# Kernel tuning notes

Measured on AMD Instinct MI355X. Metric: run time of the kernel, lower is better.

Reference implementation:

```python
import jax, jax.numpy as jnp
import numpy as np

B, S, D, H, HD = 2, 2048, 2048, 16, 128
MAX_TIMESCALE = 10000.0


def _fixed_pos_embedding(features, length, max_timescale):
    # flaxformer embedding.generate_fixed_pos_embedding
    fraction = jnp.arange(0, features, 2, dtype=jnp.float32) / features
    timescale = max_timescale ** fraction  # min_timescale = 1.0
    sinusoid = jnp.einsum('i,j->ij', jnp.arange(length, dtype=jnp.float32), 1.0 / timescale)
    sinusoid = jnp.concatenate([sinusoid, sinusoid], axis=-1)  # [length, features]
    return jnp.sin(sinusoid), jnp.cos(sinusoid)


def _rotate_half(x):
    x1, x2 = jnp.split(x, 2, axis=-1)
    return jnp.concatenate([-x2, x1], axis=-1)


def _apply_rope(x, sin, cos):
    # x: [B, S, H, HD]; sin/cos: [S, HD]
    sin = sin[None, :, None, :].astype(x.dtype)
    cos = cos[None, :, None, :].astype(x.dtype)
    return x * cos + _rotate_half(x) * sin


def setup_inputs() -> dict:
    key = jax.random.key(0)
    ks = jax.random.split(key, 6)
    inputs_q = jax.random.normal(ks[0], (B, S, D), dtype=jnp.float32)
    inputs_kv = jax.random.normal(ks[1], (B, S, D), dtype=jnp.float32)
    scale = D ** -0.5
    wq = jax.random.normal(ks[2], (D, H, HD), dtype=jnp.float32) * scale
    wk = jax.random.normal(ks[3], (D, H, HD), dtype=jnp.float32) * scale
    wv = jax.random.normal(ks[4], (D, H, HD), dtype=jnp.float32) * scale
    wo = jax.random.normal(ks[5], (H, HD, D), dtype=jnp.float32) * ((H * HD) ** -0.5)
    mask = jnp.tril(jnp.ones((S, S), dtype=bool))[None, None]  # causal [1,1,S,S]
    return {"inputs_q": inputs_q, "inputs_kv": inputs_kv, "wq": wq, "wk": wk,
            "wv": wv, "wo": wo, "mask": mask}


def reference(inputs_q, inputs_kv, wq, wk, wv, wo, mask):
    # QKV projections (split-head kernels) -> [B, S, H, HD]
    q = jnp.einsum('bqd,dhf->bqhf', inputs_q, wq)
    k = jnp.einsum('bkd,dhf->bkhf', inputs_kv, wk)
    v = jnp.einsum('bkd,dhf->bkhf', inputs_kv, wv)

    # Rotary embeddings applied to full head dim (fraction_to_rotate = 1.0)
    sin, cos = _fixed_pos_embedding(HD, S, MAX_TIMESCALE)
    q = _apply_rope(q, sin, cos)
    k = _apply_rope(k, sin, cos)

    # Logit rescaling by 1/sqrt(head_dim) (rescale_logits=False default path)
    q = q * (HD ** -0.5)

    logits = jnp.einsum('bqhf,bkhf->bhqk', q, k)  # [B, H, S, S]
    logits = jnp.where(mask, logits, jnp.asarray(-1e10, logits.dtype))
    probs = jax.nn.softmax(logits, axis=-1)

    ctx = jnp.einsum('bhqk,bkhf->bqhf', probs, v)
    out = jnp.einsum('bqhf,hfd->bqd', ctx, wo)  # output projection
    return out
```

## Files before the change

### kernel.cpp

```cpp
#include <hip/hip_runtime.h>

#define S_LEN 2048
#define NH 16
#define HDIM 128
#define DMODEL 2048

typedef __attribute__((ext_vector_type(8))) short bf16x8;
typedef __attribute__((ext_vector_type(4))) float f32x4;

using gas_cvp = const __attribute__((address_space(1))) void*;
using las_vp  = __attribute__((address_space(3))) void*;

__device__ __forceinline__ unsigned short f2bf(float x) {
  unsigned int u = __builtin_bit_cast(unsigned int, x);
  u += 0x7FFFu + ((u >> 16) & 1u);
  return (unsigned short)(u >> 16);
}
__device__ __forceinline__ float bf2f(unsigned short u) {
  unsigned int x = ((unsigned int)u) << 16;
  return __builtin_bit_cast(float, x);
}
__device__ __forceinline__ unsigned int cvt_pk_bf16(float lo, float hi) {
  unsigned int r;
  asm("v_cvt_pk_bf16_f32 %0, %1, %2" : "=v"(r) : "v"(lo), "v"(hi));
  return r;
}

__global__ __launch_bounds__(256) void cvt2_kernel(const float4* __restrict__ inq,
                                                   const float4* __restrict__ inkv,
                                                   ushort4* __restrict__ outq,
                                                   ushort4* __restrict__ outkv, int n4) {
  const float4* in = blockIdx.z ? inkv : inq;
  ushort4* out = blockIdx.z ? outkv : outq;
  int i = blockIdx.x * 256 + threadIdx.x;
  if (i < n4) {
    float4 v = in[i];
    ushort4 r;
    r.x = f2bf(v.x); r.y = f2bf(v.y); r.z = f2bf(v.z); r.w = f2bf(v.w);
    out[i] = r;
  }
}

__global__ __launch_bounds__(256) void sincos_kernel(float2* __restrict__ sc) {
  int i = blockIdx.x * 256 + threadIdx.x;
  int s = i >> 6, j = i & 63;
  float inv_ts = 1.0f / powf(10000.0f, (float)j * (1.0f / 64.0f));
  float ang = (float)s * inv_ts;
  sc[i] = make_float2(sinf(ang), cosf(ang));
}

__global__ __launch_bounds__(256) void rope8_kernel(const unsigned short* __restrict__ XQ,
                                                    const unsigned short* __restrict__ XK,
                                                    const float2* __restrict__ sc,
                                                    unsigned short* __restrict__ outQ,
                                                    unsigned short* __restrict__ outK,
                                                    float qscale) {
  const unsigned short* X = blockIdx.z ? XK : XQ;
  unsigned short* out = blockIdx.z ? outK : outQ;
  float scale = blockIdx.z ? 1.0f : qscale;
  int i = blockIdx.x * 256 + threadIdx.x;
  int m = i >> 7;
  int r = i & 127;
  int h = r >> 3, jb = (r & 7) * 8;
  int s = m & (S_LEN - 1);
  size_t base = (size_t)m * DMODEL + h * HDIM + jb;
  int4 x1 = *(const int4*)(X + base);
  int4 x2 = *(const int4*)(X + base + 64);
  const float2* pp = sc + s * 64 + jb;
  int4 o1, o2;
  int* x1w = (int*)&x1; int* x2w = (int*)&x2;
  int* o1w = (int*)&o1; int* o2w = (int*)&o2;
#pragma unroll
  for (int w = 0; w < 4; w++) {
    float a_lo = bf2f((unsigned short)(x1w[w] & 0xffff));
    float a_hi = bf2f((unsigned short)((unsigned int)x1w[w] >> 16));
    float b_lo = bf2f((unsigned short)(x2w[w] & 0xffff));
    float b_hi = bf2f((unsigned short)((unsigned int)x2w[w] >> 16));
    float2 c0 = pp[w * 2], c1 = pp[w * 2 + 1];
    float r1l = (a_lo * c0.y - b_lo * c0.x) * scale;
    float r1h = (a_hi * c1.y - b_hi * c1.x) * scale;
    float r2l = (b_lo * c0.y + a_lo * c0.x) * scale;
    float r2h = (b_hi * c1.y + a_hi * c1.x) * scale;
    o1w[w] = (int)(cvt_pk_bf16(r1l, r1h));
    o2w[w] = (int)(cvt_pk_bf16(r2l, r2h));
  }
  *(int4*)(out + base) = o1;
  *(int4*)(out + base + 64) = o2;
}

__global__ __launch_bounds__(256) void wtrans4_kernel(const float* __restrict__ w0,
                                                      const float* __restrict__ w1,
                                                      const float* __restrict__ w2,
                                                      const float* __restrict__ w3,
                                                      unsigned short* __restrict__ outb) {
  __shared__ float tile[64][65];
  int z = blockIdx.z;
  const float* in = (z == 0) ? w0 : (z == 1) ? w1 : (z == 2) ? w2 : w3;
  unsigned short* out = outb + (size_t)z * DMODEL * DMODEL;
  int c0 = blockIdx.x * 64, r0 = blockIdx.y * 64;
  int tx = threadIdx.x & 63, ty = threadIdx.x >> 6;
#pragma unroll
  for (int i = 0; i < 16; i++) {
    int r = ty + i * 4;
    tile[r][tx] = in[(size_t)(r0 + r) * DMODEL + c0 + tx];
  }
  __syncthreads();
#pragma unroll
  for (int i = 0; i < 16; i++) {
    int c = ty + i * 4;
    out[(size_t)(c0 + c) * DMODEL + r0 + tx] = f2bf(tile[tx][c]);
  }
}

__global__ __launch_bounds__(256) void vtrans_kernel(const unsigned short* __restrict__ vf,
                                                     unsigned short* __restrict__ Vt) {
  __shared__ unsigned short tile[64][65];
  int z = blockIdx.z; int b = z >> 4, h = z & 15;
  const unsigned short* I = vf + (size_t)b * S_LEN * DMODEL + h * HDIM;
  unsigned short* O = Vt + (size_t)z * HDIM * S_LEN;
  int s0 = blockIdx.y * 64, f0 = blockIdx.x * 64;
  int tx = threadIdx.x & 63, ty = threadIdx.x >> 6;
#pragma unroll
  for (int i = 0; i < 16; i++) {
    int r = ty + i * 4;
    tile[r][tx] = I[(size_t)(s0 + r) * DMODEL + f0 + tx];
  }
  __syncthreads();
#pragma unroll
  for (int i = 0; i < 16; i++) {
    int c = ty + i * 4;
    O[(size_t)(f0 + c) * S_LEN + s0 + tx] = tile[tx][c];
  }
}

__global__ __launch_bounds__(512, 1) void gemm256o_kernel(
    const unsigned short* __restrict__ Aq,
    const unsigned short* __restrict__ Akv,
    const unsigned short* __restrict__ W,
    unsigned short* __restrict__ Cb) {
  constexpr int M = 4096, N = 2048, K = 2048, NT = K / 64;
  __shared__ char lds[131072];
  int wid = blockIdx.z * 128 + blockIdx.y * 8 + blockIdx.x;
  int nid = (wid & 7) * 32 + (wid >> 3);
  int z = nid >> 7;
  int rem = nid & 127;
  int bm = (rem >> 3) * 256, bn = (rem & 7) * 256;
  const unsigned short* A = (z == 0) ? Aq : Akv;
  const unsigned short* Bt = W + (size_t)z * N * K;

  int tid = threadIdx.x, wave = tid >> 6, lane = tid & 63;
  int lr = lane & 15, lq = lane >> 4;
  int wr = wave >> 2, wc = wave & 3;

  auto STAGE_P = [&](int t, int buf, int isB) {
    int k0 = t * 64;
    const unsigned short* src = isB ? Bt : A;
    int rbase = isB ? bn : bm;
    char* dst0 = lds + buf * 65536 + isB * 32768;
#pragma unroll
    for (int i = 0; i < 4; i++) {
      int o = i * 8192 + tid * 16;
      int row = o >> 7, colb = o & 127;
      int sc = colb ^ ((row & 7) << 4);
      __builtin_amdgcn_global_load_lds(
          (gas_cvp)(src + (size_t)(rbase + row) * K + k0 + (sc >> 1)),
          (las_vp)(dst0 + i * 8192 + wave * 1024), 16, 0, 0);
    }
  };
  auto LDA1 = [&](int buf, int m, int kk) -> bf16x8 {
    int row = wr * 128 + m * 16 + lr;
    return *(const bf16x8*)(lds + buf * 65536 + row * 128 +
                            (((kk * 4 + lq) ^ (row & 7)) << 4));
  };
  auto LDB1 = [&](int buf, int n, int kk) -> bf16x8 {
    int row = wc * 64 + n * 16 + lr;
    return *(const bf16x8*)(lds + buf * 65536 + 32768 + row * 128 +
                            (((kk * 4 + lq) ^ (row & 7)) << 4));
  };

  f32x4 acc[8][4] = {};
  bf16x8 aA[4][2], bB[4][2];

  auto OCT = [&](int P, int Q, int sb) {
#pragma unroll
    for (int kk = 0; kk < 2; kk++)
#pragma unroll
      for (int s = 0; s < 2; s++)
#pragma unroll
        for (int nn = 0; nn < 2; nn++)
          acc[2 * P + s][2 * Q + nn] = __builtin_amdgcn_mfma_f32_16x16x32_bf16(
              aA[sb + s][kk], bB[2 * Q + nn][kk], acc[2 * P + s][2 * Q + nn], 0, 0, 0);
  };
  auto RD_A2 = [&](int buf, int m0, int sb) {
#pragma unroll
    for (int kk = 0; kk < 2; kk++)
#pragma unroll
      for (int s = 0; s < 2; s++) aA[sb + s][kk] = LDA1(buf, m0 + s, kk);
  };
  auto RD_B2 = [&](int buf, int n0) {
#pragma unroll
    for (int kk = 0; kk < 2; kk++)
#pragma unroll
      for (int s = 0; s < 2; s++) bB[n0 + s][kk] = LDB1(buf, n0 + s, kk);
  };

  STAGE_P(0, 0, 0); STAGE_P(0, 0, 1);
  asm volatile("s_waitcnt vmcnt(0)" ::: "memory");
  __builtin_amdgcn_sched_barrier(0);

  for (int T = 0; T < NT; T++) {
    int c = T & 1, nc = c ^ 1;
    __builtin_amdgcn_s_barrier();
    if (T + 1 < NT) { STAGE_P(T + 1, nc, 0); STAGE_P(T + 1, nc, 1); }
    __builtin_amdgcn_sched_barrier(0);
    RD_A2(c, 0, 0);
    __builtin_amdgcn_sched_barrier(0);
    RD_B2(c, 0);
    __builtin_amdgcn_sched_barrier(0);
    RD_B2(c, 2);
    __builtin_amdgcn_sched_barrier(0);
    RD_A2(c, 2, 2);
    __builtin_amdgcn_sched_barrier(0);

    asm volatile("s_waitcnt lgkmcnt(8)" ::: "memory");
    __builtin_amdgcn_sched_barrier(0);
    __builtin_amdgcn_s_setprio(1);
    OCT(0, 0, 0);
    __builtin_amdgcn_s_setprio(0);
    asm volatile("s_waitcnt lgkmcnt(4)" ::: "memory");
    __builtin_amdgcn_sched_barrier(0);
    __builtin_amdgcn_s_setprio(1);
    OCT(0, 1, 0);
    __builtin_amdgcn_s_setprio(0);
    RD_A2(c, 4, 0);
    __builtin_amdgcn_sched_barrier(0);
    asm volatile("s_waitcnt lgkmcnt(4)" ::: "memory");
    __builtin_amdgcn_sched_barrier(0);
    __builtin_amdgcn_s_setprio(1);
    OCT(1, 0, 2); OCT(1, 1, 2);
    __builtin_amdgcn_s_setprio(0);
    RD_A2(c, 6, 2);
    __builtin_amdgcn_sched_barrier(0);
    asm volatile("s_waitcnt lgkmcnt(4)" ::: "memory");
    __builtin_amdgcn_sched_barrier(0);
    __builtin_amdgcn_s_setprio(1);
    OCT(2, 0, 0); OCT(2, 1, 0);
    __builtin_amdgcn_s_setprio(0);
    asm volatile("s_waitcnt lgkmcnt(0)" ::: "memory");
    __builtin_amdgcn_sched_barrier(0);
    __builtin_amdgcn_s_setprio(1);
    OCT(3, 0, 2); OCT(3, 1, 2);
    __builtin_amdgcn_s_setprio(0);
    if (T + 1 < NT) {
      asm volatile("s_waitcnt vmcnt(0)" ::: "memory");
      __builtin_amdgcn_sched_barrier(0);
    }
  }
  asm volatile("s_waitcnt vmcnt(0) lgkmcnt(0)" ::: "memory");

  unsigned short* C = Cb + (size_t)z * M * N;
#pragma unroll
  for (int m = 0; m < 8; m++)
#pragma unroll
    for (int n = 0; n < 4; n++) {
      int row0 = bm + wr * 128 + m * 16 + lq * 4;
      int col = bn + wc * 64 + n * 16 + lr;
#pragma unroll
      for (int r = 0; r < 4; r++)
        C[(size_t)(row0 + r) * N + col] = f2bf(acc[m][n][r]);
    }
}

template <bool BF16OUT>
__global__ __launch_bounds__(512, 1) void gemmk_kernel(
    const unsigned short* __restrict__ Aq,
    const unsigned short* __restrict__ Akv,
    const unsigned short* __restrict__ W,
    void* __restrict__ Cb) {
  constexpr int M = 4096, N = 2048, K = 2048, NT = K / 64;
  __shared__ char lds[147456];
  int z = blockIdx.z;
  const unsigned short* A = (z == 0) ? Aq : Akv;
  const unsigned short* Bt = W + (size_t)z * N * K;

  int wid = blockIdx.y * 16 + blockIdx.x;
  int nid = (wid & 7) * 32 + (wid >> 3);
  int bn = (nid & 15) * 128, bm = (nid >> 4) * 256;

  int tid = threadIdx.x, wave = tid >> 6, lane = tid & 63;
  int lr = lane & 15, lq = lane >> 4;
  int wr = wave >> 1, wc = wave & 1;

  auto STAGE_U = [&](int t, int buf, int which) {
    int k0 = t * 64;
    const unsigned short* src = (which < 2) ? A : Bt;
    int rbase = (which < 2) ? (bm + which * 128) : bn;
    char* dst0 = lds + buf * 49152 + which * 16384;
#pragma unroll
    for (int i = 0; i < 2; i++) {
      int o = i * 8192 + wave * 1024 + lane * 16;
      int row = o >> 7, colb = o & 127;
      int sc = colb ^ ((row & 7) << 4);
      __builtin_amdgcn_global_load_lds(
          (gas_cvp)(src + (size_t)(rbase + row) * K + k0 + (sc >> 1)),
          (las_vp)(dst0 + i * 8192 + wave * 1024), 16, 0, 0);
    }
  };
  auto LDA = [&](int buf, int m, int kk) -> bf16x8 {
    int row = wr * 64 + m * 16 + lr;
    int half = row >> 7, r = row & 127;
    int byt = r * 128 + (((kk * 4 + lq) ^ (r & 7)) << 4);
    return *(const bf16x8*)(lds + buf * 49152 + half * 16384 + byt);
  };
  auto LDB = [&](int buf, int n, int kk) -> bf16x8 {
    int row = wc * 64 + n * 16 + lr;
    int byt = row * 128 + (((kk * 4 + lq) ^ (row & 7)) << 4);
    return *(const bf16x8*)(lds + buf * 49152 + 32768 + byt);
  };

  f32x4 acc[4][4] = {};
  bf16x8 aA[4][2], bB[4][2];

  auto QUAD = [&](int mg, int ng) {
#pragma unroll
    for (int kk = 0; kk < 2; kk++)
#pragma unroll
      for (int mm = 0; mm < 2; mm++)
#pragma unroll
        for (int nn = 0; nn < 2; nn++)
          acc[mg * 2 + mm][ng * 2 + nn] = __builtin_amdgcn_mfma_f32_16x16x32_bf16(
              aA[mg * 2 + mm][kk], bB[ng * 2 + nn][kk], acc[mg * 2 + mm][ng * 2 + nn], 0, 0, 0);
  };

  auto BODY = [&](int T, int cur, int dst, int mode) {
    __builtin_amdgcn_s_barrier();
    if (mode == 0) {
      STAGE_U(T + 2, dst, 0); STAGE_U(T + 2, dst, 1); STAGE_U(T + 2, dst, 2);
    }
    __builtin_amdgcn_sched_barrier(0);
#pragma unroll
    for (int kk = 0; kk < 2; kk++)
#pragma unroll
      for (int mm = 0; mm < 2; mm++) aA[mm][kk] = LDA(cur, mm, kk);
#pragma unroll
    for (int kk = 0; kk < 2; kk++)
#pragma unroll
      for (int nn = 0; nn < 2; nn++) bB[nn][kk] = LDB(cur, nn, kk);
    __builtin_amdgcn_sched_barrier(0);
#pragma unroll
    for (int kk = 0; kk < 2; kk++)
#pragma unroll
      for (int nn = 0; nn < 2; nn++) bB[2 + nn][kk] = LDB(cur, 2 + nn, kk);
    __builtin_amdgcn_sched_barrier(0);
#pragma unroll
    for (int kk = 0; kk < 2; kk++)
#pragma unroll
      for (int mm = 0; mm < 2; mm++) aA[2 + mm][kk] = LDA(cur, 2 + mm, kk);
    __builtin_amdgcn_sched_barrier(0);

    asm volatile("s_waitcnt lgkmcnt(8)" ::: "memory");
    __builtin_amdgcn_sched_barrier(0);
    __builtin_amdgcn_s_setprio(1);
    QUAD(0, 0);
    __builtin_amdgcn_s_setprio(0);
    asm volatile("s_waitcnt lgkmcnt(4)" ::: "memory");
    __builtin_amdgcn_sched_barrier(0);
    __builtin_amdgcn_s_setprio(1);
    QUAD(0, 1);
    __builtin_amdgcn_s_setprio(0);
    asm volatile("s_waitcnt lgkmcnt(0)" ::: "memory");
    __builtin_amdgcn_sched_barrier(0);
    __builtin_amdgcn_s_setprio(1);
    QUAD(1, 0); QUAD(1, 1);
    __builtin_amdgcn_s_setprio(0);
    if (mode == 0)      asm volatile("s_waitcnt vmcnt(6)" ::: "memory");
    else if (mode == 1) asm volatile("s_waitcnt vmcnt(0)" ::: "memory");
    __builtin_amdgcn_sched_barrier(0);
  };

  STAGE_U(0, 0, 0); STAGE_U(0, 0, 1); STAGE_U(0, 0, 2);
  STAGE_U(1, 1, 0); STAGE_U(1, 1, 1); STAGE_U(1, 1, 2);
  asm volatile("s_waitcnt vmcnt(6)" ::: "memory");
  __builtin_amdgcn_sched_barrier(0);

  int cur = 0;
  for (int T = 0; T < NT - 2; T++) {
    int dst = (cur == 0) ? 2 : cur - 1;
    BODY(T, cur, dst, 0);
    cur = (cur == 2) ? 0 : cur + 1;
  }
  BODY(NT - 2, cur, 0, 1);
  cur = (cur == 2) ? 0 : cur + 1;
  BODY(NT - 1, cur, 0, 2);
  asm volatile("s_waitcnt vmcnt(0) lgkmcnt(0)" ::: "memory");

#pragma unroll
  for (int m = 0; m < 4; m++)
#pragma unroll
    for (int n = 0; n < 4; n++) {
      int row0 = bm + wr * 64 + m * 16 + lq * 4;
      int col = bn + wc * 64 + n * 16 + lr;
      if (BF16OUT) {
        unsigned short* C = (unsigned short*)Cb;
#pragma unroll
        for (int r = 0; r < 4; r++)
          C[(size_t)(row0 + r) * N + col] = f2bf(acc[m][n][r]);
      } else {
        float* C = (float*)Cb;
#pragma unroll
        for (int r = 0; r < 4; r++)
          C[(size_t)(row0 + r) * N + col] = acc[m][n][r];
      }
    }
}

__global__ __launch_bounds__(512, 1) void attn_kernel(const unsigned short* __restrict__ Qb,
                                                      const unsigned short* __restrict__ Kb,
                                                      const unsigned short* __restrict__ Vt,
                                                      unsigned short* __restrict__ ctx) {
  __shared__ char lds[65536];
  int d = blockIdx.x + 8 * (blockIdx.y + 16 * blockIdx.z);
  int jlo = (d >> 3) & 7;
  int hb = (d & 7) * 4 + (d >> 6);
  int h = hb & 15, b = hb >> 4;

  int tid = threadIdx.x, wave = tid >> 6, lane = tid & 63;
  int lr = lane & 15, lq = lane >> 4;
  int grp = wave >> 2, wsub = wave & 3;
  int qtile = grp ? (15 - jlo) : jlo;
  int qw = qtile * 128 + wsub * 32;
  int nt = 2 * (15 - jlo) + 2;

  const unsigned short* Qp = Qb + (size_t)b * S_LEN * DMODEL + (size_t)h * HDIM;
  const unsigned short* Kp = Kb + (size_t)b * S_LEN * DMODEL + (size_t)h * HDIM;
  const unsigned short* Vp = Vt + (size_t)(b * NH + h) * HDIM * S_LEN;

  bf16x8 qa[2][4];
#pragma unroll
  for (int mi = 0; mi < 2; mi++)
#pragma unroll
    for (int kf = 0; kf < 4; kf++)
      qa[mi][kf] = *(const bf16x8*)(Qp + (size_t)(qw + mi * 16 + lr) * DMODEL + kf * 32 + lq * 8);

  f32x4 o[2][8] = {};
  float mrow[2] = {-1e30f, -1e30f};
  float lsum[2] = {0.f, 0.f};

  auto STAGE = [&](int tt, int bsel) {
    int kk0 = tt * 64;
#pragma unroll
    for (int i = 0; i < 2; i++) {
      int o_ = wave * 2048 + i * 1024 + lane * 16;
      int row = o_ >> 8, colb = o_ & 255;
      int sc_ = colb ^ ((row & 7) << 4);
      __builtin_amdgcn_global_load_lds(
          (gas_cvp)(Kp + (size_t)(kk0 + row) * DMODEL + (sc_ >> 1)),
          (las_vp)(lds + bsel * 32768 + wave * 2048 + i * 1024), 16, 0, 0);
    }
#pragma unroll
    for (int i = 0; i < 2; i++) {
      int o_ = wave * 2048 + i * 1024 + lane * 16;
      int row = o_ >> 7, colb = o_ & 127;
      int sc_ = colb ^ ((row & 7) << 4);
      __builtin_amdgcn_global_load_lds(
          (gas_cvp)(Vp + (size_t)row * S_LEN + kk0 + (sc_ >> 1)),
          (las_vp)(lds + bsel * 32768 + 16384 + wave * 2048 + i * 1024), 16, 0, 0);
    }
  };

  STAGE(0, 0);
  __syncthreads();

  for (int t = 0; t < nt; t++) {
    int cur = t & 1;
    int k0 = t * 64;
    if (t + 1 < nt) STAGE(t + 1, cur ^ 1);

    bool active = (k0 <= qw + 31);
    if (active) {
      const char* kbb = lds + cur * 32768;
      f32x4 sf[2][4] = {};
#pragma unroll
      for (int kf = 0; kf < 4; kf++) {
        bf16x8 kbf[4];
#pragma unroll
        for (int nf = 0; nf < 4; nf++) {
          int row = nf * 16 + lr;
          int colb = kf * 64 + lq * 16;
          kbf[nf] = *(const bf16x8*)(kbb + row * 256 + (colb ^ ((row & 7) << 4)));
        }
#pragma unroll
        for (int nf = 0; nf < 4; nf++)
#pragma unroll
          for (int mi = 0; mi < 2; mi++)
            sf[mi][nf] = __builtin_amdgcn_mfma_f32_16x16x32_bf16(kbf[nf], qa[mi][kf], sf[mi][nf], 0, 0, 0);
      }

      if (k0 + 63 > qw) {
#pragma unroll
        for (int mi = 0; mi < 2; mi++) {
          int q = qw + mi * 16 + lr;
#pragma unroll
          for (int nf = 0; nf < 4; nf++)
#pragma unroll
            for (int r = 0; r < 4; r++)
              if (k0 + nf * 16 + lq * 4 + r > q) sf[mi][nf][r] = -1e30f;
        }
      }

      float vmax[2];
#pragma unroll
      for (int mi = 0; mi < 2; mi++) {
        float v = sf[mi][0][0];
#pragma unroll
        for (int nf = 0; nf < 4; nf++)
#pragma unroll
          for (int r = 0; r < 4; r++) v = fmaxf(v, sf[mi][nf][r]);
        v = fmaxf(v, __shfl_xor(v, 16));
        v = fmaxf(v, __shfl_xor(v, 32));
        vmax[mi] = v;
      }
      bool need = (vmax[0] > mrow[0] + 8.f) || (vmax[1] > mrow[1] + 8.f);
      if (__any(need)) {
#pragma unroll
        for (int mi = 0; mi < 2; mi++) {
          float mn = fmaxf(mrow[mi], vmax[mi]);
          float al = __expf(mrow[mi] - mn);
          mrow[mi] = mn;
          lsum[mi] *= al;
#pragma unroll
          for (int ff = 0; ff < 8; ff++) o[mi][ff] *= al;
        }
      }
#pragma unroll
      for (int mi = 0; mi < 2; mi++) {
        float rs = 0.f;
#pragma unroll
        for (int nf = 0; nf < 4; nf++)
#pragma unroll
          for (int r = 0; r < 4; r++) {
            float p = __expf(sf[mi][nf][r] - mrow[mi]);
            sf[mi][nf][r] = p;
            rs += p;
          }
        rs += __shfl_xor(rs, 16);
        rs += __shfl_xor(rs, 32);
        lsum[mi] += rs;
      }

      const char* vbb = lds + cur * 32768 + 16384;
      bool hi = (lane >= 32);
      bool odd = (lq & 1);
#pragma unroll
      for (int c = 0; c < 2; c++) {
        bf16x8 pfrag[2];
#pragma unroll
        for (int mi = 0; mi < 2; mi++) {
          unsigned int A0 = cvt_pk_bf16(sf[mi][2 * c][0], sf[mi][2 * c][1]);
          unsigned int A1 = cvt_pk_bf16(sf[mi][2 * c][2], sf[mi][2 * c][3]);
          unsigned int B0 = cvt_pk_bf16(sf[mi][2 * c + 1][0], sf[mi][2 * c + 1][1]);
          unsigned int B1 = cvt_pk_bf16(sf[mi][2 * c + 1][2], sf[mi][2 * c + 1][3]);
          unsigned int sA0 = (unsigned int)__shfl_xor((int)A0, 32);
          unsigned int sA1 = (unsigned int)__shfl_xor((int)A1, 32);
          unsigned int sB0 = (unsigned int)__shfl_xor((int)B0, 32);
          unsigned int sB1 = (unsigned int)__shfl_xor((int)B1, 32);
          unsigned int Y0f = hi ? sB0 : A0, Y0s = hi ? B0 : sA0;
          unsigned int Y1f = hi ? sB1 : A1, Y1s = hi ? B1 : sA1;
          unsigned int z0 = odd ? Y0f : Y0s, z1 = odd ? Y1f : Y1s;
          unsigned int w0 = (unsigned int)__shfl_xor((int)z0, 16);
          unsigned int w1 = (unsigned int)__shfl_xor((int)z1, 16);
          int4 fr;
          fr.x = (int)(odd ? w0 : Y0f);
          fr.y = (int)(odd ? w1 : Y1f);
          fr.z = (int)(odd ? Y0s : w0);
          fr.w = (int)(odd ? Y1s : w1);
          pfrag[mi] = __builtin_bit_cast(bf16x8, fr);
        }
#pragma unroll
        for (int ff = 0; ff < 8; ff++) {
          int row = ff * 16 + lr;
          int colb = c * 64 + lq * 16;
          bf16x8 vb = *(const bf16x8*)(vbb + row * 128 + (colb ^ ((row & 7) << 4)));
#pragma unroll
          for (int mi = 0; mi < 2; mi++)
            o[mi][ff] = __builtin_amdgcn_mfma_f32_16x16x32_bf16(vb, pfrag[mi], o[mi][ff], 0, 0, 0);
        }
      }
    }

    __syncthreads();
  }

#pragma unroll
  for (int mi = 0; mi < 2; mi++) {
    float inv = 1.0f / lsum[mi];
    size_t rb = ((size_t)b * S_LEN + qw + mi * 16 + lr) * DMODEL + h * HDIM;
#pragma unroll
    for (int ff = 0; ff < 8; ff++) {
      unsigned int u0 = cvt_pk_bf16(o[mi][ff][0] * inv, o[mi][ff][1] * inv);
      unsigned int u1 = cvt_pk_bf16(o[mi][ff][2] * inv, o[mi][ff][3] * inv);
      *(uint2*)(ctx + rb + ff * 16 + lq * 4) = make_uint2(u0, u1);
    }
  }
}

extern "C" void kernel_launch(void* const* d_in, const int* in_sizes, int n_in,
                              void* d_out, int out_size, void* d_ws, size_t ws_size,
                              hipStream_t stream) {
  const float* inq  = (const float*)d_in[0];
  const float* inkv = (const float*)d_in[1];
  const float* wq   = (const float*)d_in[2];
  const float* wk   = (const float*)d_in[3];
  const float* wv   = (const float*)d_in[4];
  const float* wo   = (const float*)d_in[5];
  float* out = (float*)d_out;

  char* ws = (char*)d_ws;
  const size_t MB = 1ull << 20;
  unsigned short* xq  = (unsigned short*)(ws);
  unsigned short* xkv = (unsigned short*)(ws + 16 * MB);
  unsigned short* wqt = (unsigned short*)(ws + 32 * MB);
  unsigned short* wvt = (unsigned short*)(ws + 48 * MB);
  unsigned short* wot = (unsigned short*)(ws + 56 * MB);
  float2* sc          = (float2*)(ws + 64 * MB);
  unsigned short* projb = (unsigned short*)(ws + 66 * MB);
  unsigned short* Vt   = (unsigned short*)(ws + 114 * MB);
  unsigned short* ctxb = (unsigned short*)(ws + 130 * MB);
  unsigned short* Qb = xq;
  unsigned short* Kb = xkv;

  const int n4 = (2 * S_LEN * DMODEL) / 4;
  cvt2_kernel<<<dim3(n4 / 256, 1, 2), 256, 0, stream>>>(
      (const float4*)inq, (const float4*)inkv, (ushort4*)xq, (ushort4*)xkv, n4);

  wtrans4_kernel<<<dim3(32, 32, 4), 256, 0, stream>>>(wq, wk, wv, wo, wqt);

  sincos_kernel<<<(S_LEN * 64) / 256, 256, 0, stream>>>(sc);

  const float qscale = 0.08838834764831845f;
  unsigned short* projQ = projb;
  unsigned short* projK = projb + (size_t)4096 * 2048;
  unsigned short* projV = projb + (size_t)2 * 4096 * 2048;

  gemm256o_kernel<<<dim3(8, 16, 2), 512, 0, stream>>>(xq, xkv, wqt, projb);
  gemmk_kernel<true><<<dim3(16, 16, 1), 512, 0, stream>>>(xkv, xkv, wvt, (void*)projV);

  rope8_kernel<<<dim3(2048, 1, 2), 256, 0, stream>>>(projQ, projK, sc, Qb, Kb, qscale);
  vtrans_kernel<<<dim3(2, 32, 32), 256, 0, stream>>>(projV, Vt);

  attn_kernel<<<dim3(8, NH, 2), 512, 0, stream>>>(Qb, Kb, Vt, ctxb);

  gemmk_kernel<false><<<dim3(16, 16, 1), 512, 0, stream>>>(ctxb, ctxb, wot, (void*)out);
}
```

Before: 264.3 us.

## Split attention into one 128-row query tile per block with longest-first ordering

Measured after the change: 259.5 us. About the same (-1.8%).

```diff
diff --git a/kernel.cpp b/kernel.cpp
--- a/kernel.cpp
+++ b/kernel.cpp
@@ -414,37 +414,36 @@
     }
 }
 
-__global__ __launch_bounds__(512, 1) void attn_kernel(const unsigned short* __restrict__ Qb,
+__global__ __launch_bounds__(512, 4) void attn_kernel(const unsigned short* __restrict__ Qb,
                                                       const unsigned short* __restrict__ Kb,
                                                       const unsigned short* __restrict__ Vt,
                                                       unsigned short* __restrict__ ctx) {
   __shared__ char lds[65536];
-  int d = blockIdx.x + 8 * (blockIdx.y + 16 * blockIdx.z);
-  int jlo = (d >> 3) & 7;
-  int hb = (d & 7) * 4 + (d >> 6);
+  int d = blockIdx.x;
+  int hb = d & 31;
+  int rank = d >> 5;
+  int qtile = (rank < 8) ? (15 - rank) : (rank - 8);
   int h = hb & 15, b = hb >> 4;
 
   int tid = threadIdx.x, wave = tid >> 6, lane = tid & 63;
   int lr = lane & 15, lq = lane >> 4;
-  int grp = wave >> 2, wsub = wave & 3;
-  int qtile = grp ? (15 - jlo) : jlo;
-  int qw = qtile * 128 + wsub * 32;
-  int nt = 2 * (15 - jlo) + 2;
+  int qw = qtile * 128 + wave * 16;
+  int nt = 2 * qtile + 2;
 
   const unsigned short* Qp = Qb + (size_t)b * S_LEN * DMODEL + (size_t)h * HDIM;
   const unsigned short* Kp = Kb + (size_t)b * S_LEN * DMODEL + (size_t)h * HDIM;
   const unsigned short* Vp = Vt + (size_t)(b * NH + h) * HDIM * S_LEN;
 
-  bf16x8 qa[2][4];
-#pragma unroll
-  for (int mi = 0; mi < 2; mi++)
-#pragma unroll
-    for (int kf = 0; kf < 4; kf++)
-      qa[mi][kf] = *(const bf16x8*)(Qp + (size_t)(qw + mi * 16 + lr) * DMODEL + kf * 32 + lq * 8);
-
-  f32x4 o[2][8] = {};
-  float mrow[2] = {-1e30f, -1e30f};
-  float lsum[2] = {0.f, 0.f};
+  bf16x8 qa[4];
+#pragma unroll
+  for (int kf = 0; kf < 4; kf++)
+    qa[kf] = *(const bf16x8*)(Qp + (size_t)(qw + lr) * DMODEL + kf * 32 + lq * 8);
+
+  f32x4 o[8] = {};
+  float mrow = -1e30f;
+  float lsum = 0.f;
+  bool hi = (lane >= 32);
+  bool odd = (lq & 1);
 
   auto STAGE = [&](int tt, int bsel) {
     int kk0 = tt * 64;
@@ -476,10 +475,10 @@
     int k0 = t * 64;
     if (t + 1 < nt) STAGE(t + 1, cur ^ 1);
 
-    bool active = (k0 <= qw + 31);
+    bool active = (k0 <= qw + 15);
     if (active) {
       const char* kbb = lds + cur * 32768;
-      f32x4 sf[2][4] = {};
+      f32x4 sf[4] = {};
 #pragma unroll
       for (int kf = 0; kf < 4; kf++) {
         bf16x8 kbf[4];
@@ -491,99 +490,75 @@
         }
 #pragma unroll
         for (int nf = 0; nf < 4; nf++)
-#pragma unroll
-          for (int mi = 0; mi < 2; mi++)
-            sf[mi][nf] = __builtin_amdgcn_mfma_f32_16x16x32_bf16(kbf[nf], qa[mi][kf], sf[mi][nf], 0, 0, 0);
+          sf[nf] = __builtin_amdgcn_mfma_f32_16x16x32_bf16(kbf[nf], qa[kf], sf[nf], 0, 0, 0);
       }
 
       if (k0 + 63 > qw) {
-#pragma unroll
-        for (int mi = 0; mi < 2; mi++) {
-          int q = qw + mi * 16 + lr;
-#pragma unroll
-          for (int nf = 0; nf < 4; nf++)
-#pragma unroll
-            for (int r = 0; r < 4; r++)
-              if (k0 + nf * 16 + lq * 4 + r > q) sf[mi][nf][r] = -1e30f;
+        int q = qw + lr;
+#pragma unroll
+        for (int nf = 0; nf < 4; nf++)
+#pragma unroll
+          for (int r = 0; r < 4; r++)
+            if (k0 + nf * 16 + lq * 4 + r > q) sf[nf][r] = -1e30f;
+      }
+
+      float v = sf[0][0];
+#pragma unroll
+      for (int nf = 0; nf < 4; nf++)
+#pragma unroll
+        for (int r = 0; r < 4; r++) v = fmaxf(v, sf[nf][r]);
+      v = fmaxf(v, __shfl_xor(v, 16));
+      v = fmaxf(v, __shfl_xor(v, 32));
+      bool need = (v > mrow + 8.f);
+      if (__any(need)) {
+        float mn = fmaxf(mrow, v);
+        float al = exp2f(mrow - mn);
+        mrow = mn;
+        lsum *= al;
+#pragma unroll
+        for (int ff = 0; ff < 8; ff++) o[ff] *= al;
+      }
+      float rs = 0.f;
+#pragma unroll
+      for (int nf = 0; nf < 4; nf++)
+#pragma unroll
+        for (int r = 0; r < 4; r++) {
+          float p = exp2f(sf[nf][r] - mrow);
+          sf[nf][r] = p;
+          rs += p;
         }
-      }
-
-      float vmax[2];
-#pragma unroll
-      for (int mi = 0; mi < 2; mi++) {
-        float v = sf[mi][0][0];
-#pragma unroll
-        for (int nf = 0; nf < 4; nf++)
-#pragma unroll
-          for (int r = 0; r < 4; r++) v = fmaxf(v, sf[mi][nf][r]);
-        v = fmaxf(v, __shfl_xor(v, 16));
-        v = fmaxf(v, __shfl_xor(v, 32));
-        vmax[mi] = v;
-      }
-      bool need = (vmax[0] > mrow[0] + 8.f) || (vmax[1] > mrow[1] + 8.f);
-      if (__any(need)) {
-#pragma unroll
-        for (int mi = 0; mi < 2; mi++) {
-          float mn = fmaxf(mrow[mi], vmax[mi]);
-          float al = __expf(mrow[mi] - mn);
-          mrow[mi] = mn;
-          lsum[mi] *= al;
-#pragma unroll
-          for (int ff = 0; ff < 8; ff++) o[mi][ff] *= al;
-        }
-      }
-#pragma unroll
-      for (int mi = 0; mi < 2; mi++) {
-        float rs = 0.f;
-#pragma unroll
-        for (int nf = 0; nf < 4; nf++)
-#pragma unroll
-          for (int r = 0; r < 4; r++) {
-            float p = __expf(sf[mi][nf][r] - mrow[mi]);
-            sf[mi][nf][r] = p;
-            rs += p;
-          }
-        rs += __shfl_xor(rs, 16);
-        rs += __shfl_xor(rs, 32);
-        lsum[mi] += rs;
-      }
+      rs += __shfl_xor(rs, 16);
+      rs += __shfl_xor(rs, 32);
+      lsum += rs;
 
       const char* vbb = lds + cur * 32768 + 16384;
-      bool hi = (lane >= 32);
-      bool odd = (lq & 1);
 #pragma unroll
       for (int c = 0; c < 2; c++) {
-        bf16x8 pfrag[2];
-#pragma unroll
-        for (int mi = 0; mi < 2; mi++) {
-          unsigned int A0 = cvt_pk_bf16(sf[mi][2 * c][0], sf[mi][2 * c][1]);
-          unsigned int A1 = cvt_pk_bf16(sf[mi][2 * c][2], sf[mi][2 * c][3]);
-          unsigned int B0 = cvt_pk_bf16(sf[mi][2 * c + 1][0], sf[mi][2 * c + 1][1]);
-          unsigned int B1 = cvt_pk_bf16(sf[mi][2 * c + 1][2], sf[mi][2 * c + 1][3]);
-          unsigned int sA0 = (unsigned int)__shfl_xor((int)A0, 32);
-          unsigned int sA1 = (unsigned int)__shfl_xor((int)A1, 32);
-          unsigned int sB0 = (unsigned int)__shfl_xor((int)B0, 32);
-          unsigned int sB1 = (unsigned int)__shfl_xor((int)B1, 32);
-          unsigned int Y0f = hi ? sB0 : A0, Y0s = hi ? B0 : sA0;
-          unsigned int Y1f = hi ? sB1 : A1, Y1s = hi ? B1 : sA1;
-          unsigned int z0 = odd ? Y0f : Y0s, z1 = odd ? Y1f : Y1s;
-          unsigned int w0 = (unsigned int)__shfl_xor((int)z0, 16);
-          unsigned int w1 = (unsigned int)__shfl_xor((int)z1, 16);
-          int4 fr;
-          fr.x = (int)(odd ? w0 : Y0f);
-          fr.y = (int)(odd ? w1 : Y1f);
-          fr.z = (int)(odd ? Y0s : w0);
-          fr.w = (int)(odd ? Y1s : w1);
-          pfrag[mi] = __builtin_bit_cast(bf16x8, fr);
-        }
+        unsigned int A0 = cvt_pk_bf16(sf[2 * c][0], sf[2 * c][1]);
+        unsigned int A1 = cvt_pk_bf16(sf[2 * c][2], sf[2 * c][3]);
+        unsigned int B0 = cvt_pk_bf16(sf[2 * c + 1][0], sf[2 * c + 1][1]);
+        unsigned int B1 = cvt_pk_bf16(sf[2 * c + 1][2], sf[2 * c + 1][3]);
+        unsigned int sA0 = (unsigned int)__shfl_xor((int)A0, 32);
+        unsigned int sA1 = (unsigned int)__shfl_xor((int)A1, 32);
+        unsigned int sB0 = (unsigned int)__shfl_xor((int)B0, 32);
+        unsigned int sB1 = (unsigned int)__shfl_xor((int)B1, 32);
+        unsigned int Y0f = hi ? sB0 : A0, Y0s = hi ? B0 : sA0;
+        unsigned int Y1f = hi ? sB1 : A1, Y1s = hi ? B1 : sA1;
+        unsigned int z0 = odd ? Y0f : Y0s, z1 = odd ? Y1f : Y1s;
+        unsigned int w0 = (unsigned int)__shfl_xor((int)z0, 16);
+        unsigned int w1 = (unsigned int)__shfl_xor((int)z1, 16);
+        int4 fr;
+        fr.x = (int)(odd ? w0 : Y0f);
+        fr.y = (int)(odd ? w1 : Y1f);
+        fr.z = (int)(odd ? Y0s : w0);
+        fr.w = (int)(odd ? Y1s : w1);
+        bf16x8 pfrag = __builtin_bit_cast(bf16x8, fr);
 #pragma unroll
         for (int ff = 0; ff < 8; ff++) {
           int row = ff * 16 + lr;
           int colb = c * 64 + lq * 16;
           bf16x8 vb = *(const bf16x8*)(vbb + row * 128 + (colb ^ ((row & 7) << 4)));
-#pragma unroll
-          for (int mi = 0; mi < 2; mi++)
-            o[mi][ff] = __builtin_amdgcn_mfma_f32_16x16x32_bf16(vb, pfrag[mi], o[mi][ff], 0, 0, 0);
+          o[ff] = __builtin_amdgcn_mfma_f32_16x16x32_bf16(vb, pfrag, o[ff], 0, 0, 0);
         }
       }
     }
@@ -591,16 +566,13 @@
     __syncthreads();
   }
 
-#pragma unroll
-  for (int mi = 0; mi < 2; mi++) {
-    float inv = 1.0f / lsum[mi];
-    size_t rb = ((size_t)b * S_LEN + qw + mi * 16 + lr) * DMODEL + h * HDIM;
-#pragma unroll
-    for (int ff = 0; ff < 8; ff++) {
-      unsigned int u0 = cvt_pk_bf16(o[mi][ff][0] * inv, o[mi][ff][1] * inv);
-      unsigned int u1 = cvt_pk_bf16(o[mi][ff][2] * inv, o[mi][ff][3] * inv);
-      *(uint2*)(ctx + rb + ff * 16 + lq * 4) = make_uint2(u0, u1);
-    }
+  float inv = 1.0f / lsum;
+  size_t rb = ((size_t)b * S_LEN + qw + lr) * DMODEL + h * HDIM;
+#pragma unroll
+  for (int ff = 0; ff < 8; ff++) {
+    unsigned int u0 = cvt_pk_bf16(o[ff][0] * inv, o[ff][1] * inv);
+    unsigned int u1 = cvt_pk_bf16(o[ff][2] * inv, o[ff][3] * inv);
+    *(uint2*)(ctx + rb + ff * 16 + lq * 4) = make_uint2(u0, u1);
   }
 }
 
@@ -637,7 +609,7 @@
 
   sincos_kernel<<<(S_LEN * 64) / 256, 256, 0, stream>>>(sc);
 
-  const float qscale = 0.08838834764831845f;
+  const float qscale = 0.12751743249052045f;
   unsigned short* projQ = projb;
   unsigned short* projK = projb + (size_t)4096 * 2048;
   unsigned short* projV = projb + (size_t)2 * 4096 * 2048;
@@ -648,7 +620,7 @@
   rope8_kernel<<<dim3(2048, 1, 2), 256, 0, stream>>>(projQ, projK, sc, Qb, Kb, qscale);
   vtrans_kernel<<<dim3(2, 32, 32), 256, 0, stream>>>(projV, Vt);
 
-  attn_kernel<<<dim3(8, NH, 2), 512, 0, stream>>>(Qb, Kb, Vt, ctxb);
+  attn_kernel<<<512, 512, 0, stream>>>(Qb, Kb, Vt, ctxb);
 
   gemmk_kernel<false><<<dim3(16, 16, 1), 512, 0, stream>>>(ctxb, ctxb, wot, (void*)out);
 }
```
